# Kernel optimization log

Hardware: AMD Instinct MI355X
Metric: run time of the kernel (lower is better)

Reference implementation:

```python
import jax, jax.numpy as jnp
import numpy as np

N, IN, OUT, H = 8192, 128, 64, 4
NEG_SLOPE = 0.2   # GATConv leaky-relu slope
EPS = 1e-5        # BatchNorm1d eps
MASK_VAL = -1e9   # masked_fill value for non-edges (finite for grad safety)


def setup_inputs() -> dict:
    key = jax.random.key(0)
    ks = jax.random.split(key, 5)
    x = jax.random.normal(ks[0], (N, IN), jnp.float32)
    adj = jax.random.randint(ks[1], (N, N), 0, 2, jnp.int32)  # dense 0/1 adjacency
    W = jax.random.normal(ks[2], (H, IN, OUT), jnp.float32) * (1.0 / np.sqrt(IN))
    a_i = jax.random.normal(ks[3], (H, OUT), jnp.float32) * (1.0 / np.sqrt(OUT))
    a_j = jax.random.normal(ks[4], (H, OUT), jnp.float32) * (1.0 / np.sqrt(OUT))
    gamma = jnp.ones((H * OUT,), jnp.float32)   # BN weight
    beta = jnp.zeros((H * OUT,), jnp.float32)   # BN bias
    return {"x": x, "adj": adj, "W": W, "a_i": a_i, "a_j": a_j,
            "gamma": gamma, "beta": beta}


def reference(x, adj, W, a_i, a_j, gamma, beta):
    # --- GATConv (dense adjacency, multi-head, concat) ---
    h = jnp.einsum('ni,hio->hno', x, W)              # [H, N, OUT]
    ei = jnp.einsum('hno,ho->hn', h, a_i)            # [H, N] source scores
    ej = jnp.einsum('hno,ho->hn', h, a_j)            # [H, N] target scores
    coe = ei[:, :, None] + ej[:, None, :]            # [H, N, N]
    coe = jnp.where(coe >= 0, coe, NEG_SLOPE * coe)  # leaky_relu
    coe = jnp.where(adj[None, :, :] == 0, MASK_VAL, coe)
    att = jax.nn.softmax(coe, axis=-1)               # segment softmax over neighbors
    out = jnp.einsum('hnm,hmo->hno', att, h)         # weighted aggregation
    out = jnp.transpose(out, (1, 0, 2)).reshape(N, H * OUT)  # concat heads
    # --- BatchNorm1d (training-mode batch stats over nodes) ---
    mean = jnp.mean(out, axis=0)
    var = jnp.var(out, axis=0)
    out = (out - mean) * jax.lax.rsqrt(var + EPS) * gamma + beta
    # --- ReLU ---
    return jax.nn.relu(out)
```

## Files before the change

### kernel.cpp

```cpp
#include <hip/hip_runtime.h>
#include <hip/hip_bf16.h>

#define NN   8192
#define IND  128
#define OUTD 64
#define NH   4
#define NEG_SLOPE 0.2f
#define BN_EPS 1e-5f

typedef __attribute__((ext_vector_type(8))) short bf16x8;
typedef __attribute__((ext_vector_type(4))) float f32x4;
typedef __attribute__((ext_vector_type(4))) int   i32x4;

static __device__ __forceinline__ short f2bf(float f) {
    union { float f; unsigned u; } v; v.f = f;
    return (short)((v.u + 0x8000u) >> 16);
}

__global__ __launch_bounds__(256) void k0_repackW(const float* __restrict__ W,
                                                  short* __restrict__ WB) {
    int tid = blockIdx.x * 256 + threadIdx.x;
    int o = tid & 63, i = (tid >> 6) & 127, h = tid >> 13;
    WB[((h * 16 + (i >> 3)) * 64 + o) * 8 + (i & 7)] = f2bf(W[(h * 128 + i) * 64 + o]);
}

__global__ __launch_bounds__(256) void k1_feat(const float* __restrict__ x,
                                               const short* __restrict__ WB,
                                               const float* __restrict__ a_i,
                                               const float* __restrict__ a_j,
                                               short* __restrict__ hB,
                                               float* __restrict__ t_Ri,
                                               unsigned int* __restrict__ tE12) {
    int w = threadIdx.x >> 6;
    int l = threadIdx.x & 63;
    int quad = l >> 4, lx = l & 15;
    int rb = blockIdx.x;

    f32x4 acc[4] = {};
#pragma unroll
    for (int ks = 0; ks < 4; ++ks) {
        const float* xp = x + (rb * 16 + lx) * IND + ks * 32 + quad * 8;
        f32x4 xa = *(const f32x4*)xp;
        f32x4 xb = *(const f32x4*)(xp + 4);
        bf16x8 af;
#pragma unroll
        for (int j = 0; j < 4; ++j) { af[j] = f2bf(xa[j]); af[4 + j] = f2bf(xb[j]); }
#pragma unroll
        for (int ot = 0; ot < 4; ++ot) {
            bf16x8 bf = *(const bf16x8*)(WB + ((w * 16 + ks * 4 + quad) * 64 + ot * 16 + lx) * 8);
            acc[ot] = __builtin_amdgcn_mfma_f32_16x16x32_bf16(af, bf, acc[ot], 0, 0, 0);
        }
    }
    float aiv[4], ajv[4];
#pragma unroll
    for (int ot = 0; ot < 4; ++ot) {
        aiv[ot] = a_i[w * 64 + ot * 16 + lx];
        ajv[ot] = a_j[w * 64 + ot * 16 + lx];
    }
#pragma unroll
    for (int reg = 0; reg < 4; ++reg) {
        int row = rb * 16 + quad * 4 + reg;
        float ei = 0.f, ej = 0.f;
#pragma unroll
        for (int ot = 0; ot < 4; ++ot) {
            float hv = acc[ot][reg];
            ei += hv * aiv[ot];
            ej += hv * ajv[ot];
        }
#pragma unroll
        for (int m = 1; m <= 8; m <<= 1) {
            ei += __shfl_xor(ei, m, 64);
            ej += __shfl_xor(ej, m, 64);
        }
        if (lx == reg) {
            t_Ri[w * NN + row] = expf(-0.8f * ei);
            unsigned e1 = (unsigned)(unsigned short)f2bf(expf(ej));
            unsigned e2 = (unsigned)(unsigned short)f2bf(expf(NEG_SLOPE * ej));
            tE12[w * NN + row] = (e2 << 16) | e1;
        }
#pragma unroll
        for (int ot = 0; ot < 4; ++ot) {
            int o = ot * 16 + lx;
            hB[((w * 1024 + (row >> 3)) * 64 + o) * 8 + (row & 7)] = f2bf(acc[ot][reg]);
        }
    }
}

__global__ __launch_bounds__(256) void k2_attn(const int* __restrict__ adj,
                                               const short* __restrict__ hB,
                                               const float* __restrict__ t_Ri,
                                               const unsigned int* __restrict__ tE12,
                                               float* __restrict__ num,
                                               float* __restrict__ Lsum) {
    __shared__ unsigned char smask[64 * 260];
    int tid = threadIdx.x;
    int w = tid >> 6;
    int l = tid & 63;
    int quad = l >> 4, lx = l & 15;
    int rb = blockIdx.x >> 2, ks = blockIdx.x & 3;
    int rowbase = rb * 64;
    int tb = w * NN;
    int k0 = ks * 2048;

    {
        int kc = tid * 8;
#pragma unroll 4
        for (int i = 0; i < 64; ++i) {
            const int* ap = adj + (size_t)(rowbase + i) * NN + k0 + kc;
            i32x4 a0 = *(const i32x4*)ap;
            i32x4 a1 = *(const i32x4*)(ap + 4);
            unsigned m = 0;
#pragma unroll
            for (int j = 0; j < 4; ++j) {
                m |= (a0[j] ? 1u : 0u) << j;
                m |= (a1[j] ? 1u : 0u) << (4 + j);
            }
            smask[i * 260 + tid] = (unsigned char)m;
        }
    }
    __syncthreads();

    float Riv[4];
    int mrow[4];
#pragma unroll
    for (int r = 0; r < 4; ++r) {
        Riv[r] = t_Ri[tb + rowbase + r * 16 + lx];
        mrow[r] = (r * 16 + lx) * 260 + quad;
    }

    bf16x8 onesf;
#pragma unroll
    for (int j = 0; j < 8; ++j) onesf[j] = (short)0x3F80;

    f32x4 acc[4][4] = {};
    f32x4 accL[4] = {};
    i32x4 pt0, pt1;
    bf16x8 pbf[4];
    {
        int kb = k0 + quad * 8;
        pt0 = *(const i32x4*)(tE12 + tb + kb);
        pt1 = *(const i32x4*)(tE12 + tb + kb + 4);
#pragma unroll
        for (int ot = 0; ot < 4; ++ot)
            pbf[ot] = *(const bf16x8*)(hB + ((w * 1024 + (kb >> 3)) * 64 + ot * 16 + lx) * 8);
    }

#pragma unroll 2
    for (int kt = 0; kt < 64; ++kt) {
        i32x4 t0 = pt0, t1 = pt1;
        bf16x8 bfrag[4];
#pragma unroll
        for (int ot = 0; ot < 4; ++ot) bfrag[ot] = pbf[ot];

        int ktn = (kt + 1) & 63;
        int kbn = k0 + ktn * 32 + quad * 8;
        pt0 = *(const i32x4*)(tE12 + tb + kbn);
        pt1 = *(const i32x4*)(tE12 + tb + kbn + 4);
#pragma unroll
        for (int ot = 0; ot < 4; ++ot)
            pbf[ot] = *(const bf16x8*)(hB + ((w * 1024 + (kbn >> 3)) * 64 + ot * 16 + lx) * 8);

        int mc[4];
#pragma unroll
        for (int r = 0; r < 4; ++r) mc[r] = smask[mrow[r] + kt * 4];

        float e1v[8], e2v[8];
#pragma unroll
        for (int c = 0; c < 8; ++c) {
            unsigned wd = (unsigned)((c < 4) ? t0[c] : t1[c - 4]);
            e1v[c] = __uint_as_float(wd << 16);
            e2v[c] = __uint_as_float(wd & 0xffff0000u);
        }

        bf16x8 afr[4];
#pragma unroll
        for (int r = 0; r < 4; ++r) {
            union { i32x4 i; bf16x8 b; } af;
#pragma unroll
            for (int jj = 0; jj < 4; ++jj) {
                int j0 = 2 * jj, j1 = 2 * jj + 1;
                float p0 = fmaxf(e1v[j0], Riv[r] * e2v[j0]);
                float p1 = fmaxf(e1v[j1], Riv[r] * e2v[j1]);
                p0 = (mc[r] & (1 << j0)) ? p0 : 0.0f;
                p1 = (mc[r] & (1 << j1)) ? p1 : 0.0f;
                af.i[jj] = (int)__builtin_amdgcn_perm(__float_as_uint(p1),
                                                      __float_as_uint(p0),
                                                      0x07060302);
            }
            afr[r] = af.b;
        }
#pragma unroll
        for (int r = 0; r < 4; ++r)
            accL[r] = __builtin_amdgcn_mfma_f32_16x16x32_bf16(afr[r], onesf, accL[r], 0, 0, 0);
#pragma unroll
        for (int r = 0; r < 4; ++r)
#pragma unroll
            for (int ot = 0; ot < 4; ++ot)
                acc[r][ot] = __builtin_amdgcn_mfma_f32_16x16x32_bf16(afr[r], bfrag[ot], acc[r][ot], 0, 0, 0);
    }

#pragma unroll
    for (int r = 0; r < 4; ++r)
        if (lx == 0)
#pragma unroll
            for (int reg = 0; reg < 4; ++reg)
                atomicAdd(&Lsum[w * NN + rowbase + r * 16 + quad * 4 + reg], accL[r][reg]);
#pragma unroll
    for (int r = 0; r < 4; ++r)
#pragma unroll
        for (int ot = 0; ot < 4; ++ot)
#pragma unroll
            for (int reg = 0; reg < 4; ++reg) {
                int row = rowbase + r * 16 + quad * 4 + reg;
                atomicAdd(&num[row * 256 + w * 64 + ot * 16 + lx], acc[r][ot][reg]);
            }
}

__global__ __launch_bounds__(256) void k3_stats(const float* __restrict__ num,
                                                const float* __restrict__ Lsum,
                                                float* __restrict__ stats) {
    int c = threadIdx.x;
    int h = c >> 6;
    float s = 0.f, s2 = 0.f;
#pragma unroll
    for (int rr = 0; rr < 8; ++rr) {
        int row = blockIdx.x * 8 + rr;
        float val = num[row * 256 + c] / Lsum[h * NN + row];
        s += val; s2 += val * val;
    }
    atomicAdd(&stats[c], s);
    atomicAdd(&stats[c + 256], s2);
}

__global__ __launch_bounds__(256) void k5_apply(const float* __restrict__ num,
                                                const float* __restrict__ Lsum,
                                                const float* __restrict__ stats,
                                                const float* __restrict__ gamma,
                                                const float* __restrict__ beta,
                                                float* __restrict__ out) {
    __shared__ float sbnp[512];
    int c = threadIdx.x;
    float mean = stats[c] * (1.0f / NN);
    float var  = stats[c + 256] * (1.0f / NN) - mean * mean;
    float sc = gamma[c] * rsqrtf(var + BN_EPS);
    sbnp[c] = sc;
    sbnp[c + 256] = beta[c] - mean * sc;
    __syncthreads();

    int g = blockIdx.x * 256 + threadIdx.x;
    f32x4 v = *(const f32x4*)(num + (size_t)g * 4);
    int cb = (g * 4) & 255;
    int row = g >> 6;
    float rL = 1.0f / Lsum[(cb >> 6) * NN + row];
    f32x4 r;
#pragma unroll
    for (int j = 0; j < 4; ++j)
        r[j] = fmaxf((v[j] * rL) * sbnp[cb + j] + sbnp[256 + cb + j], 0.0f);
    *(f32x4*)(out + (size_t)g * 4) = r;
}

extern "C" void kernel_launch(void* const* d_in, const int* in_sizes, int n_in,
                              void* d_out, int out_size, void* d_ws, size_t ws_size,
                              hipStream_t stream) {
    (void)in_sizes; (void)n_in; (void)out_size; (void)ws_size;
    const float* x     = (const float*)d_in[0];
    const int*   adj   = (const int*)d_in[1];
    const float* W     = (const float*)d_in[2];
    const float* a_i   = (const float*)d_in[3];
    const float* a_j   = (const float*)d_in[4];
    const float* gamma = (const float*)d_in[5];
    const float* beta  = (const float*)d_in[6];
    float* out = (float*)d_out;

    char* ws = (char*)d_ws;
    short*        WB    = (short*)(ws + 0);
    short*        hB    = (short*)(ws + 65536);
    float*        t_Ri  = (float*)(ws + 4259840);
    unsigned int* tE12  = (unsigned int*)(ws + 4390912);
    float*        num   = (float*)(ws + 4521984);
    float*        Lsum  = (float*)(ws + 12910592);
    float*        stats = (float*)(ws + 13041664);

    hipMemsetAsync(num, 0, 8388608 + 131072 + 2048, stream);

    k0_repackW<<<dim3(128),  dim3(256), 0, stream>>>(W, WB);
    k1_feat   <<<dim3(512),  dim3(256), 0, stream>>>(x, WB, a_i, a_j, hB, t_Ri, tE12);
    k2_attn   <<<dim3(512),  dim3(256), 0, stream>>>(adj, hB, t_Ri, tE12, num, Lsum);
    k3_stats  <<<dim3(1024), dim3(256), 0, stream>>>(num, Lsum, stats);
    k5_apply  <<<dim3(2048), dim3(256), 0, stream>>>(num, Lsum, stats, gamma, beta, out);
}
```

Baseline: 479.5 us.

## Switch attention weights to packed fp16 math with LUT masks and finer K split

```diff
diff --git a/kernel.cpp b/kernel.cpp
--- a/kernel.cpp
+++ b/kernel.cpp
@@ -8,13 +8,20 @@
 #define NEG_SLOPE 0.2f
 #define BN_EPS 1e-5f
 
-typedef __attribute__((ext_vector_type(8))) short bf16x8;
-typedef __attribute__((ext_vector_type(4))) float f32x4;
-typedef __attribute__((ext_vector_type(4))) int   i32x4;
+typedef __attribute__((ext_vector_type(8))) short     bf16x8;
+typedef __attribute__((ext_vector_type(8))) _Float16  f16x8;
+typedef __attribute__((ext_vector_type(2))) _Float16  h2;
+typedef __attribute__((ext_vector_type(4))) float     f32x4;
+typedef __attribute__((ext_vector_type(4))) int       i32x4;
+
+union V4 { i32x4 i; f16x8 v; };
 
 static __device__ __forceinline__ short f2bf(float f) {
     union { float f; unsigned u; } v; v.f = f;
     return (short)((v.u + 0x8000u) >> 16);
+}
+static __device__ __forceinline__ unsigned short f2h(float f) {
+    union { _Float16 h; unsigned short s; } u; u.h = (_Float16)f; return u.s;
 }
 
 __global__ __launch_bounds__(256) void k0_repackW(const float* __restrict__ W,
@@ -28,9 +35,10 @@
                                                const short* __restrict__ WB,
                                                const float* __restrict__ a_i,
                                                const float* __restrict__ a_j,
-                                               short* __restrict__ hB,
+                                               unsigned short* __restrict__ hF,
                                                float* __restrict__ t_Ri,
-                                               unsigned int* __restrict__ tE12) {
+                                               unsigned short* __restrict__ tE1,
+                                               unsigned short* __restrict__ tE2) {
     int w = threadIdx.x >> 6;
     int l = threadIdx.x & 63;
     int quad = l >> 4, lx = l & 15;
@@ -74,129 +82,137 @@
         }
         if (lx == reg) {
             t_Ri[w * NN + row] = expf(-0.8f * ei);
-            unsigned e1 = (unsigned)(unsigned short)f2bf(expf(ej));
-            unsigned e2 = (unsigned)(unsigned short)f2bf(expf(NEG_SLOPE * ej));
-            tE12[w * NN + row] = (e2 << 16) | e1;
+            tE1[w * NN + row] = f2h(expf(ej));
+            tE2[w * NN + row] = f2h(expf(NEG_SLOPE * ej));
         }
 #pragma unroll
         for (int ot = 0; ot < 4; ++ot) {
             int o = ot * 16 + lx;
-            hB[((w * 1024 + (row >> 3)) * 64 + o) * 8 + (row & 7)] = f2bf(acc[ot][reg]);
+            hF[((w * 1024 + (row >> 3)) * 64 + o) * 8 + (row & 7)] = f2h(acc[ot][reg]);
         }
     }
 }
 
 __global__ __launch_bounds__(256) void k2_attn(const int* __restrict__ adj,
-                                               const short* __restrict__ hB,
+                                               const unsigned short* __restrict__ hF,
                                                const float* __restrict__ t_Ri,
-                                               const unsigned int* __restrict__ tE12,
+                                               const unsigned short* __restrict__ tE1,
+                                               const unsigned short* __restrict__ tE2,
                                                float* __restrict__ num,
                                                float* __restrict__ Lsum) {
-    __shared__ unsigned char smask[64 * 260];
+    __shared__ unsigned char smask[128 * 68];
+    __shared__ unsigned int  lutm[256 * 4];
     int tid = threadIdx.x;
     int w = tid >> 6;
     int l = tid & 63;
     int quad = l >> 4, lx = l & 15;
-    int rb = blockIdx.x >> 2, ks = blockIdx.x & 3;
+    int rb = blockIdx.x & 127, ks = blockIdx.x >> 7;
     int rowbase = rb * 64;
     int tb = w * NN;
-    int k0 = ks * 2048;
+    int k0 = ks * 1024;
 
     {
-        int kc = tid * 8;
-#pragma unroll 4
-        for (int i = 0; i < 64; ++i) {
-            const int* ap = adj + (size_t)(rowbase + i) * NN + k0 + kc;
-            i32x4 a0 = *(const i32x4*)ap;
-            i32x4 a1 = *(const i32x4*)(ap + 4);
-            unsigned m = 0;
-#pragma unroll
-            for (int j = 0; j < 4; ++j) {
-                m |= (a0[j] ? 1u : 0u) << j;
-                m |= (a1[j] ? 1u : 0u) << (4 + j);
+        unsigned b = (unsigned)tid;
+        i32x4 e;
+#pragma unroll
+        for (int jj = 0; jj < 4; ++jj) {
+            unsigned lo = (b >> (2 * jj)) & 1u, hi = (b >> (2 * jj + 1)) & 1u;
+            e[jj] = (int)(lo * 0x3C00u + hi * 0x3C000000u);
+        }
+        *(i32x4*)&lutm[tid * 4] = e;
+    }
+
+    {
+        int cg = tid & 127, half = tid >> 7;
+        const int* abase = adj + (size_t)rowbase * NN + k0 + cg * 8;
+#pragma unroll 2
+        for (int rr = 0; rr < 8; ++rr) {
+            int rl = half * 8 + rr;
+            unsigned mword = 0;
+#pragma unroll
+            for (int rh = 0; rh < 4; ++rh) {
+                const int* ap = abase + (size_t)(rh * 16 + rl) * NN;
+                i32x4 a0 = *(const i32x4*)ap;
+                i32x4 a1 = *(const i32x4*)(ap + 4);
+                unsigned m = 0;
+#pragma unroll
+                for (int j = 0; j < 4; ++j) {
+                    m |= (a0[j] ? 1u : 0u) << j;
+                    m |= (a1[j] ? 1u : 0u) << (4 + j);
+                }
+                mword |= m << (8 * rh);
             }
-            smask[i * 260 + tid] = (unsigned char)m;
+            *(unsigned int*)&smask[cg * 68 + rl * 4] = mword;
         }
     }
     __syncthreads();
 
-    float Riv[4];
-    int mrow[4];
+    h2 Rh2[4];
 #pragma unroll
     for (int r = 0; r < 4; ++r) {
-        Riv[r] = t_Ri[tb + rowbase + r * 16 + lx];
-        mrow[r] = (r * 16 + lx) * 260 + quad;
-    }
-
-    bf16x8 onesf;
-#pragma unroll
-    for (int j = 0; j < 8; ++j) onesf[j] = (short)0x3F80;
+        _Float16 rv = (_Float16)t_Ri[tb + rowbase + r * 16 + lx];
+        Rh2[r][0] = rv; Rh2[r][1] = rv;
+    }
+
+    V4 ones;
+#pragma unroll
+    for (int jj = 0; jj < 4; ++jj) ones.i[jj] = 0x3C003C00;
 
     f32x4 acc[4][4] = {};
     f32x4 accL[4] = {};
-    i32x4 pt0, pt1;
-    bf16x8 pbf[4];
+
+    i32x4 p1, p2;
+    V4 pbf[4];
+    unsigned pm32;
     {
         int kb = k0 + quad * 8;
-        pt0 = *(const i32x4*)(tE12 + tb + kb);
-        pt1 = *(const i32x4*)(tE12 + tb + kb + 4);
+        p1 = *(const i32x4*)(tE1 + tb + kb);
+        p2 = *(const i32x4*)(tE2 + tb + kb);
 #pragma unroll
         for (int ot = 0; ot < 4; ++ot)
-            pbf[ot] = *(const bf16x8*)(hB + ((w * 1024 + (kb >> 3)) * 64 + ot * 16 + lx) * 8);
+            pbf[ot].i = *(const i32x4*)(hF + ((w * 1024 + (kb >> 3)) * 64 + ot * 16 + lx) * 8);
+        pm32 = *(const unsigned int*)&smask[quad * 68 + lx * 4];
     }
 
 #pragma unroll 2
-    for (int kt = 0; kt < 64; ++kt) {
-        i32x4 t0 = pt0, t1 = pt1;
-        bf16x8 bfrag[4];
+    for (int kt = 0; kt < 32; ++kt) {
+        i32x4 t1 = p1, t2 = p2;
+        unsigned m32 = pm32;
+        V4 bfrag[4];
 #pragma unroll
         for (int ot = 0; ot < 4; ++ot) bfrag[ot] = pbf[ot];
 
-        int ktn = (kt + 1) & 63;
+        int ktn = (kt + 1) & 31;
         int kbn = k0 + ktn * 32 + quad * 8;
-        pt0 = *(const i32x4*)(tE12 + tb + kbn);
-        pt1 = *(const i32x4*)(tE12 + tb + kbn + 4);
+        p1 = *(const i32x4*)(tE1 + tb + kbn);
+        p2 = *(const i32x4*)(tE2 + tb + kbn);
 #pragma unroll
         for (int ot = 0; ot < 4; ++ot)
-            pbf[ot] = *(const bf16x8*)(hB + ((w * 1024 + (kbn >> 3)) * 64 + ot * 16 + lx) * 8);
-
-        int mc[4];
-#pragma unroll
-        for (int r = 0; r < 4; ++r) mc[r] = smask[mrow[r] + kt * 4];
-
-        float e1v[8], e2v[8];
-#pragma unroll
-        for (int c = 0; c < 8; ++c) {
-            unsigned wd = (unsigned)((c < 4) ? t0[c] : t1[c - 4]);
-            e1v[c] = __uint_as_float(wd << 16);
-            e2v[c] = __uint_as_float(wd & 0xffff0000u);
-        }
-
-        bf16x8 afr[4];
+            pbf[ot].i = *(const i32x4*)(hF + ((w * 1024 + (kbn >> 3)) * 64 + ot * 16 + lx) * 8);
+        pm32 = *(const unsigned int*)&smask[(ktn * 4 + quad) * 68 + lx * 4];
+
+        V4 afr[4];
 #pragma unroll
         for (int r = 0; r < 4; ++r) {
-            union { i32x4 i; bf16x8 b; } af;
+            V4 mw;
+            mw.i = *(const i32x4*)&lutm[((m32 >> (8 * r)) & 0xFFu) * 4];
 #pragma unroll
             for (int jj = 0; jj < 4; ++jj) {
-                int j0 = 2 * jj, j1 = 2 * jj + 1;
-                float p0 = fmaxf(e1v[j0], Riv[r] * e2v[j0]);
-                float p1 = fmaxf(e1v[j1], Riv[r] * e2v[j1]);
-                p0 = (mc[r] & (1 << j0)) ? p0 : 0.0f;
-                p1 = (mc[r] & (1 << j1)) ? p1 : 0.0f;
-                af.i[jj] = (int)__builtin_amdgcn_perm(__float_as_uint(p1),
-                                                      __float_as_uint(p0),
-                                                      0x07060302);
+                h2 e1 = __builtin_bit_cast(h2, (unsigned)t1[jj]);
+                h2 e2 = __builtin_bit_cast(h2, (unsigned)t2[jj]);
+                h2 mk = __builtin_bit_cast(h2, (unsigned)mw.i[jj]);
+                h2 p  = __builtin_elementwise_max(e1, Rh2[r] * e2) * mk;
+                afr[r].i[jj] = (int)__builtin_bit_cast(unsigned, p);
             }
-            afr[r] = af.b;
         }
 #pragma unroll
         for (int r = 0; r < 4; ++r)
-            accL[r] = __builtin_amdgcn_mfma_f32_16x16x32_bf16(afr[r], onesf, accL[r], 0, 0, 0);
+            accL[r] = __builtin_amdgcn_mfma_f32_16x16x32_f16(afr[r].v, ones.v, accL[r], 0, 0, 0);
 #pragma unroll
         for (int r = 0; r < 4; ++r)
 #pragma unroll
             for (int ot = 0; ot < 4; ++ot)
-                acc[r][ot] = __builtin_amdgcn_mfma_f32_16x16x32_bf16(afr[r], bfrag[ot], acc[r][ot], 0, 0, 0);
+                acc[r][ot] = __builtin_amdgcn_mfma_f32_16x16x32_f16(afr[r].v, bfrag[ot].v, acc[r][ot], 0, 0, 0);
     }
 
 #pragma unroll
@@ -273,19 +289,20 @@
     float* out = (float*)d_out;
 
     char* ws = (char*)d_ws;
-    short*        WB    = (short*)(ws + 0);
-    short*        hB    = (short*)(ws + 65536);
-    float*        t_Ri  = (float*)(ws + 4259840);
-    unsigned int* tE12  = (unsigned int*)(ws + 4390912);
-    float*        num   = (float*)(ws + 4521984);
-    float*        Lsum  = (float*)(ws + 12910592);
-    float*        stats = (float*)(ws + 13041664);
-
-    hipMemsetAsync(num, 0, 8388608 + 131072 + 2048, stream);
+    short*          WB    = (short*)(ws + 0);
+    unsigned short* hF    = (unsigned short*)(ws + 65536);
+    float*          t_Ri  = (float*)(ws + 4259840);
+    unsigned short* tE1   = (unsigned short*)(ws + 4390912);
+    unsigned short* tE2   = (unsigned short*)(ws + 4456448);
+    float*          num   = (float*)(ws + 4521984);
+    float*          Lsum  = (float*)(ws + 12910592);
+    float*          stats = (float*)(ws + 13041664);
+
+    (void)hipMemsetAsync(num, 0, 8388608 + 131072 + 2048, stream);
 
     k0_repackW<<<dim3(128),  dim3(256), 0, stream>>>(W, WB);
-    k1_feat   <<<dim3(512),  dim3(256), 0, stream>>>(x, WB, a_i, a_j, hB, t_Ri, tE12);
-    k2_attn   <<<dim3(512),  dim3(256), 0, stream>>>(adj, hB, t_Ri, tE12, num, Lsum);
+    k1_feat   <<<dim3(512),  dim3(256), 0, stream>>>(x, WB, a_i, a_j, hF, t_Ri, tE1, tE2);
+    k2_attn   <<<dim3(1024), dim3(256), 0, stream>>>(adj, hF, t_Ri, tE1, tE2, num, Lsum);
     k3_stats  <<<dim3(1024), dim3(256), 0, stream>>>(num, Lsum, stats);
     k5_apply  <<<dim3(2048), dim3(256), 0, stream>>>(num, Lsum, stats, gamma, beta, out);
 }
```

Measured after the change: 481.7 us (median of 3 runs). Within noise of the previous version (+0.5%).
